# Performance work log

Measured on AMD Instinct MI355X. Metric: run time of the kernel, lower is better.

The kernel has to match this reference:

```python
import jax, jax.numpy as jnp
import numpy as np


def setup_inputs() -> dict:
    key = jax.random.key(0)
    ks = jax.random.split(key, 9)
    b, m, e, d = 4, 4096, 2048, 256
    s = 1.0 / np.sqrt(d)
    return {
        "features": jax.random.normal(ks[0], (b, m, d), jnp.float32),
        "inc_mat": (jax.random.uniform(ks[1], (b, m, e)) < 0.05).astype(jnp.float32),
        "vc_W_att": jax.random.normal(ks[2], (d, d), jnp.float32) * s,
        "vc_W_proj": jax.random.normal(ks[3], (d, d), jnp.float32) * s,
        "vc_alpha": jnp.float32(0.5),
        "ec_W_att": jax.random.normal(ks[4], (d, d), jnp.float32) * s,
        "ec_W_proj": jax.random.normal(ks[5], (d, d), jnp.float32) * s,
        "ec_alpha": jnp.float32(0.5),
        "n_layers": 3,
    }


def _vertex_conv(feat, inc, W_att, W_proj, alpha, prev_edge):
    # feat: [b,m,d], inc: [b,m,e]
    node_scores = jnp.einsum('bmd,kd->bmk', feat, W_att)          # attention Linear (x @ W.T)
    edge_scores = jnp.einsum('bme,bmd->bed', inc, node_scores)    # inc^T @ scores
    attn = jax.nn.softmax(edge_scores, axis=1)                    # softmax over edge dim (dim=1 in torch)
    # einsum('bme,bmd->bmed') then ('bmed,bed->bed') == attn * (inc^T @ feat); no 4D intermediate
    agg = jnp.einsum('bme,bmd->bed', inc, feat)
    ef = jnp.einsum('bed,kd->bek', attn * agg, W_proj)
    if prev_edge is not None:
        ef = alpha * prev_edge + (1.0 - alpha) * ef
    return ef


def _edge_conv(inc, edge_feats, W_proj, alpha, prev_node):
    # note: EdgeConv's attention softmax is computed but unused in the original forward
    weighted = jnp.einsum('bed,bme->bmd', edge_feats, inc)        # scatter edges back to nodes
    nf = jnp.einsum('bmd,kd->bmk', weighted, W_proj)
    if prev_node is not None:
        nf = alpha * prev_node + (1.0 - alpha) * nf
    return nf


def reference(features, inc_mat, vc_W_att, vc_W_proj, vc_alpha, ec_W_att, ec_W_proj, ec_alpha, n_layers):
    edge_feats = _vertex_conv(features, inc_mat, vc_W_att, vc_W_proj, vc_alpha, None)
    node_feats = _edge_conv(inc_mat, edge_feats, ec_W_proj, ec_alpha, features)
    for _ in range(1, int(n_layers)):
        edge_feats = _vertex_conv(features, inc_mat, vc_W_att, vc_W_proj, vc_alpha, edge_feats)
        node_feats = _edge_conv(inc_mat, edge_feats, ec_W_proj, ec_alpha, node_feats)
    return (node_feats, edge_feats, inc_mat)
```

## Files before the change

### kernel.cpp

```cpp
#include <hip/hip_runtime.h>
#include <hip/hip_bf16.h>
#include <math.h>

typedef __attribute__((ext_vector_type(8))) short s8v;
typedef __attribute__((ext_vector_type(4))) float f32x4;

__device__ __forceinline__ ushort f2bf(float x){ __hip_bfloat16 h = __float2bfloat16(x); return *(ushort*)&h; }
__device__ __forceinline__ float  bf2f(ushort u){ return __bfloat162float(*(__hip_bfloat16*)&u); }

template<int MAP> __device__ __forceinline__ int kmap(int k){
  if constexpr (MAP==0) return k;
  else if constexpr (MAP==1) return k & 4095;
  else if constexpr (MAP==3) return (((k>>8)&1)<<8) | (k&255);
  else if constexpr (MAP==4) return k & 255;
  else return (((k>>9)&1)<<8) | (k&255);
}

template<int AMAP, int BMAP, int EPI, int FR>
__global__ __launch_bounds__(256)
void gemm_kernel(const ushort* __restrict__ A, int lda, long long sA,
                 const ushort* __restrict__ B, int ldb, long long sB,
                 void* __restrict__ Cp, void* __restrict__ Cp2,
                 int ldc, long long sC, int ldc2, long long sC2,
                 long long kpC, int Kloc, int kparts,
                 const float* __restrict__ blend,
                 const float* __restrict__ alpha_p, const int* __restrict__ L_p)
{
  constexpr int BMt = 32*FR;
  __shared__ ushort As[BMt][40];
  __shared__ ushort Bs[BMt][40];

  const int z  = blockIdx.z;
  const int b  = z / kparts;
  const int kp = z - b*kparts;
  const int kbase = kp * Kloc;
  A += (size_t)b * sA;
  B += (size_t)b * sB;
  const int m0 = blockIdx.x * BMt;
  const int n0 = blockIdx.y * BMt;
  const int t = threadIdx.x, lane = t & 63, wid = t >> 6;
  const int wr = (wid>>1)*(16*FR), wc = (wid&1)*(16*FR);
  const int lrow = lane & 15, koff = (lane>>4)<<3;

  f32x4 acc[FR][FR];
  #pragma unroll
  for (int i=0;i<FR;i++)
    #pragma unroll
    for (int j=0;j<FR;j++) acc[i][j] = (f32x4)(0.f);

  for (int k0 = 0; k0 < Kloc; k0 += 32) {
    if constexpr (FR==4) {
      const int row = t>>1, cb = (t&1)*16;
      { const ushort* s = A + (size_t)(m0+row)*lda + kmap<AMAP>(kbase+k0+cb);
        *(s8v*)&As[row][cb] = *(const s8v*)s; *(s8v*)&As[row][cb+8] = *(const s8v*)(s+8); }
      { const ushort* s = B + (size_t)(n0+row)*ldb + kmap<BMAP>(kbase+k0+cb);
        *(s8v*)&Bs[row][cb] = *(const s8v*)s; *(s8v*)&Bs[row][cb+8] = *(const s8v*)(s+8); }
    } else {
      const int row = t>>2, cb = (t&3)*8;
      *(s8v*)&As[row][cb] = *(const s8v*)(A + (size_t)(m0+row)*lda + kmap<AMAP>(kbase+k0+cb));
      *(s8v*)&Bs[row][cb] = *(const s8v*)(B + (size_t)(n0+row)*ldb + kmap<BMAP>(kbase+k0+cb));
    }
    __syncthreads();
    s8v af[FR], bfv[FR];
    #pragma unroll
    for (int mi=0; mi<FR; mi++) af[mi]  = *(const s8v*)&As[wr+mi*16+lrow][koff];
    #pragma unroll
    for (int ni=0; ni<FR; ni++) bfv[ni] = *(const s8v*)&Bs[wc+ni*16+lrow][koff];
    #pragma unroll
    for (int mi=0; mi<FR; mi++)
      #pragma unroll
      for (int ni=0; ni<FR; ni++)
        acc[mi][ni] = __builtin_amdgcn_mfma_f32_16x16x32_bf16(af[mi], bfv[ni], acc[mi][ni], 0,0,0);
    __syncthreads();
  }

  float aL = 0.f;
  if constexpr (EPI==2) { aL = powf(*alpha_p, (float)(*L_p)); }
  const int cr = (lane>>4)<<2, cc = lane & 15;
  #pragma unroll
  for (int mi=0; mi<FR; mi++)
    #pragma unroll
    for (int ni=0; ni<FR; ni++) {
      const int row0 = m0 + wr + mi*16 + cr;
      const int col  = n0 + wc + ni*16 + cc;
      if constexpr (EPI==0) {
        float* C = (float*)Cp + kp*kpC + (size_t)b*sC;
        #pragma unroll
        for (int r=0;r<4;r++) C[(size_t)(row0+r)*ldc + col] = acc[mi][ni][r];
      } else if constexpr (EPI==1) {
        ushort* C = (ushort*)Cp + (size_t)b*sC;
        #pragma unroll
        for (int r=0;r<4;r++) C[(size_t)(row0+r)*ldc + col] = f2bf(acc[mi][ni][r]);
      } else if constexpr (EPI==2) {
        float* C = (float*)Cp + (size_t)b*sC;
        const float* bl = blend + (size_t)b*sC;
        #pragma unroll
        for (int r=0;r<4;r++) {
          const size_t idx = (size_t)(row0+r)*ldc + col;
          C[idx] = aL*bl[idx] + (1.f-aL)*acc[mi][ni][r];
        }
      } else if constexpr (EPI==6) {
        float* C = (float*)Cp + (size_t)b*sC;
        #pragma unroll
        for (int r=0;r<4;r++) C[(size_t)(row0+r)*ldc + col] = acc[mi][ni][r];
        float* C2 = (float*)Cp2 + (size_t)b*sC2 + (size_t)col*ldc2 + row0;
        *(f32x4*)C2 = acc[mi][ni];
      } else {
        float* C = (float*)Cp + (size_t)b*sC;
        #pragma unroll
        for (int r=0;r<4;r++) C[(size_t)(row0+r)*ldc + col] = acc[mi][ni][r];
        ushort4 o;
        o.x = f2bf(acc[mi][ni][0]); o.y = f2bf(acc[mi][ni][1]);
        o.z = f2bf(acc[mi][ni][2]); o.w = f2bf(acc[mi][ni][3]);
        *(ushort4*)((ushort*)Cp2 + (size_t)b*sC2 + (size_t)col*ldc2 + row0) = o;
      }
    }
}

__global__ __launch_bounds__(256)
void trans_inc_kernel(const float* __restrict__ src, float* __restrict__ outF32, int writeF32,
                      ushort* __restrict__ incbf, ushort* __restrict__ incT)
{
  __shared__ ushort T[64][65];
  const int b = blockIdx.z, m0 = blockIdx.x*64, e0 = blockIdx.y*64;
  const int t = threadIdx.x, rl = t>>2, cl = (t&3)*16;
  const size_t roff = (size_t)b*4096*2048 + (size_t)(m0+rl)*2048 + e0 + cl;
  const float* s = src + roff;
  ushort tmp[16] __attribute__((aligned(16)));
  float4 vv[4];
  #pragma unroll
  for (int i=0;i<4;i++) {
    vv[i] = ((const float4*)s)[i];
    tmp[4*i+0]=f2bf(vv[i].x); tmp[4*i+1]=f2bf(vv[i].y);
    tmp[4*i+2]=f2bf(vv[i].z); tmp[4*i+3]=f2bf(vv[i].w);
  }
  if (writeF32) {
    float4* o = (float4*)(outF32 + roff);
    #pragma unroll
    for (int i=0;i<4;i++) o[i] = vv[i];
  }
  ushort* d = incbf + roff;
  *(s8v*)d = *(s8v*)&tmp[0]; *(s8v*)(d+8) = *(s8v*)&tmp[8];
  #pragma unroll
  for (int j=0;j<16;j++) T[rl][cl+j] = tmp[j];
  __syncthreads();
  const int er = t>>2, mc = (t&3)*16;
  ushort o[16] __attribute__((aligned(16)));
  #pragma unroll
  for (int j=0;j<16;j++) o[j] = T[mc+j][er];
  ushort* d2 = incT + (size_t)b*2048*4096 + (size_t)(e0+er)*4096 + m0 + mc;
  *(s8v*)d2 = *(s8v*)&o[0]; *(s8v*)(d2+8) = *(s8v*)&o[8];
}

__global__ __launch_bounds__(256)
void trans_feat_kernel(const float* __restrict__ feat, ushort* __restrict__ fT)
{
  __shared__ ushort Th[64][65], Tl[64][65];
  const int b = blockIdx.z, m0 = blockIdx.x*64, d0 = blockIdx.y*64;
  const int t = threadIdx.x, rl = t>>2, cl = (t&3)*16;
  const float* s = feat + (size_t)b*4096*256 + (size_t)(m0+rl)*256 + d0 + cl;
  #pragma unroll
  for (int i=0;i<4;i++) {
    float4 v = ((const float4*)s)[i];
    float a[4] = {v.x,v.y,v.z,v.w};
    #pragma unroll
    for (int j=0;j<4;j++) {
      ushort h = f2bf(a[j]); Th[rl][cl+4*i+j] = h; Tl[rl][cl+4*i+j] = f2bf(a[j] - bf2f(h));
    }
  }
  __syncthreads();
  const int dr = t>>2, mc = (t&3)*16;
  ushort oh[16] __attribute__((aligned(16)));
  ushort ol[16] __attribute__((aligned(16)));
  #pragma unroll
  for (int j=0;j<16;j++) { oh[j] = Th[mc+j][dr]; ol[j] = Tl[mc+j][dr]; }
  ushort* d2 = fT + (size_t)b*256*8192 + (size_t)(d0+dr)*8192 + m0 + mc;
  *(s8v*)d2 = *(s8v*)&oh[0]; *(s8v*)(d2+8) = *(s8v*)&oh[8];
  *(s8v*)(d2+4096) = *(s8v*)&ol[0]; *(s8v*)(d2+4104) = *(s8v*)&ol[8];
}

__global__ __launch_bounds__(256)
void cvt_w_kernel(const float4* __restrict__ W, ushort* __restrict__ Ws)
{
  size_t i  = (size_t)blockIdx.x * 256 + threadIdx.x;
  size_t e0 = i * 4;
  int c = (int)(e0 & 255), r = (int)(e0 >> 8);
  float4 v = W[i];
  float a[4] = {v.x,v.y,v.z,v.w};
  ushort* hi = Ws + (size_t)r*512 + c;
  #pragma unroll
  for (int j=0;j<4;j++) { ushort h = f2bf(a[j]); hi[j] = h; hi[256+j] = f2bf(a[j]-bf2f(h)); }
}

__global__ __launch_bounds__(256)
void aggsum_kernel(const float* __restrict__ parts, long long kpC, int kparts,
                   ushort* __restrict__ AGGcat)
{
  const size_t i4 = (size_t)blockIdx.x*256 + threadIdx.x;
  float4 sv = make_float4(0.f,0.f,0.f,0.f);
  for (int kp=0; kp<kparts; kp++) {
    float4 v = ((const float4*)(parts + (size_t)kp*kpC))[i4];
    sv.x+=v.x; sv.y+=v.y; sv.z+=v.z; sv.w+=v.w;
  }
  const size_t flat = i4*4;
  const size_t row = flat >> 8;
  const int d = (int)(flat & 255);
  float a[4] = {sv.x, sv.y, sv.z, sv.w};
  ushort4 hi, lo;
  { ushort h=f2bf(a[0]); hi.x=h; lo.x=f2bf(a[0]-bf2f(h)); }
  { ushort h=f2bf(a[1]); hi.y=h; lo.y=f2bf(a[1]-bf2f(h)); }
  { ushort h=f2bf(a[2]); hi.z=h; lo.z=f2bf(a[2]-bf2f(h)); }
  { ushort h=f2bf(a[3]); hi.w=h; lo.w=f2bf(a[3]-bf2f(h)); }
  ushort* dst = AGGcat + row*512 + d;
  *(ushort4*)dst = hi; *(ushort4*)(dst+256) = lo;
}

__global__ __launch_bounds__(256)
void stats_kernel(const float* __restrict__ ESt, float2* __restrict__ stats)
{
  const int b = blockIdx.x >> 8, d = blockIdx.x & 255;
  const float* base = ESt + ((size_t)b*256 + d)*2048;
  const int t = threadIdx.x;
  const float4* p = (const float4*)base + t*2;
  float4 x = p[0], y = p[1];
  float v[8] = {x.x,x.y,x.z,x.w,y.x,y.y,y.z,y.w};
  float mx = v[0];
  #pragma unroll
  for (int j=1;j<8;j++) mx = fmaxf(mx, v[j]);
  #pragma unroll
  for (int off=32; off>=1; off>>=1) mx = fmaxf(mx, __shfl_down(mx, off));
  __shared__ float sm[8];
  const int lane = t & 63, w = t >> 6;
  if (lane==0) sm[w] = mx;
  __syncthreads();
  if (t==0) { sm[4] = fmaxf(fmaxf(sm[0],sm[1]),fmaxf(sm[2],sm[3])); }
  __syncthreads();
  mx = sm[4];
  float s = 0.f;
  #pragma unroll
  for (int j=0;j<8;j++) s += __expf(v[j]-mx);
  #pragma unroll
  for (int off=32; off>=1; off>>=1) s += __shfl_down(s, off);
  if (lane==0) sm[w] = s;
  __syncthreads();
  if (t==0) { float ss = sm[0]+sm[1]+sm[2]+sm[3]; stats[blockIdx.x] = make_float2(mx, 1.f/ss); }
}

__global__ __launch_bounds__(256)
void pmul_kernel(const float* __restrict__ ES, const ushort* __restrict__ AGGcat,
                 const float2* __restrict__ stats, ushort* __restrict__ P)
{
  const int b = blockIdx.x >> 6, e0 = (blockIdx.x & 63) * 32;
  const int t = threadIdx.x, tx = t & 63, ty = t >> 6;
  const int d4 = tx*4;
  const float2 st0 = stats[b*256+d4+0], st1 = stats[b*256+d4+1];
  const float2 st2 = stats[b*256+d4+2], st3 = stats[b*256+d4+3];
  for (int e = e0+ty; e < e0+32; e += 4) {
    const size_t ro = (size_t)b*2048 + e;
    float4 es = *(const float4*)(ES + ro*256 + d4);
    ushort4 ah = *(const ushort4*)(AGGcat + ro*512 + d4);
    ushort4 al = *(const ushort4*)(AGGcat + ro*512 + 256 + d4);
    ushort4 o;
    o.x = f2bf(__expf(es.x-st0.x)*st0.y*(bf2f(ah.x)+bf2f(al.x)));
    o.y = f2bf(__expf(es.y-st1.x)*st1.y*(bf2f(ah.y)+bf2f(al.y)));
    o.z = f2bf(__expf(es.z-st2.x)*st2.y*(bf2f(ah.z)+bf2f(al.z)));
    o.w = f2bf(__expf(es.w-st3.x)*st3.y*(bf2f(ah.w)+bf2f(al.w)));
    *(ushort4*)(P + ro*256 + d4) = o;
  }
}

__global__ __launch_bounds__(256)
void inc_copy_kernel(const float4* __restrict__ src, float4* __restrict__ dst, size_t n4)
{
  size_t i = (size_t)blockIdx.x*256 + threadIdx.x;
  const size_t stride = (size_t)gridDim.x*256;
  for (; i < n4; i += stride) dst[i] = src[i];
}

extern "C" void kernel_launch(void* const* d_in, const int* in_sizes, int n_in,
                              void* d_out, int out_size, void* d_ws, size_t ws_size,
                              hipStream_t stream) {
  const float* feat    = (const float*)d_in[0];
  const float* inc     = (const float*)d_in[1];
  const float* vcWatt  = (const float*)d_in[2];
  const float* vcWproj = (const float*)d_in[3];
  const float* ecWproj = (const float*)d_in[6];
  const float* ecAlpha = (const float*)d_in[7];
  const int*   nLayers = (const int*)d_in[8];

  const int Bb=4, Mm=4096, E=2048, D=256;
  const size_t nodeN = (size_t)Bb*Mm*D, edgeN = (size_t)Bb*E*D, incN = (size_t)Bb*Mm*E;

  const int kparts = 8;
  const size_t fTB    = (size_t)Bb*256*8192*2;
  const size_t partsB = (size_t)kparts*Bb*E*D*4;
  const size_t AGGcatB= (size_t)Bb*E*512*2;
  const size_t ESB    = (size_t)Bb*E*D*4;
  const size_t EStB   = ESB;
  const size_t PB     = edgeN*2;
  const size_t edgeTB = edgeN*2;
  const size_t WtB    = nodeN*2;
  const size_t WsB    = (size_t)3*256*512*2;
  const size_t statB  = (size_t)Bb*256*sizeof(float2);
  const size_t incTB  = incN*2, incbfB = incN*2;
  const size_t needB  = fTB+partsB+AGGcatB+ESB+EStB+PB+edgeTB+WtB+WsB+statB;
  const bool planA = ws_size >= needB + incTB + incbfB;

  char* ws = (char*)d_ws;
  ushort* fT    = (ushort*)ws;  ws += fTB;
  float*  parts = (float*)ws;   ws += partsB;
  ushort* AGGcat= (ushort*)ws;  ws += AGGcatB;
  float*  ES    = (float*)ws;   ws += ESB;
  float*  ESt   = (float*)ws;   ws += EStB;
  ushort* P     = (ushort*)ws;  ws += PB;
  ushort* edgeT = (ushort*)ws;  ws += edgeTB;
  ushort* Wt    = (ushort*)ws;  ws += WtB;
  ushort* Ws0   = (ushort*)ws;
  ushort* Ws1   = Ws0 + 256*512;
  ushort* Ws2   = Ws1 + 256*512;
  ws += WsB;
  float2* stats = (float2*)ws;  ws += statB;

  float* outNode = (float*)d_out;
  float* outEdge = outNode + nodeN;
  float* outInc  = outEdge + edgeN;
  ushort* incT, *incbf;
  if (planA) { incT = (ushort*)ws; incbf = incT + incN; }
  else       { incT = (ushort*)outInc; incbf = incT + incN; }

  const long long kpC = (long long)Bb*E*D;
  dim3 blk(256);

  cvt_w_kernel<<<dim3(64), blk, 0, stream>>>((const float4*)vcWatt,  Ws0);
  cvt_w_kernel<<<dim3(64), blk, 0, stream>>>((const float4*)vcWproj, Ws1);
  cvt_w_kernel<<<dim3(64), blk, 0, stream>>>((const float4*)ecWproj, Ws2);
  trans_feat_kernel<<<dim3(64,4,4), blk, 0, stream>>>(feat, fT);
  trans_inc_kernel<<<dim3(64,32,4), blk, 0, stream>>>(inc, outInc, planA ? 1 : 0, incbf, incT);

  gemm_kernel<1,0,0,4><<<dim3(16,2,4*kparts), blk, 0, stream>>>(
      incT, 4096, (long long)E*4096, fT, 8192, (long long)256*8192,
      parts, nullptr, D, (long long)E*D, 0, 0, kpC, 8192/kparts, kparts,
      nullptr, nullptr, nullptr);

  aggsum_kernel<<<dim3(2048), blk, 0, stream>>>(parts, kpC, kparts, AGGcat);

  gemm_kernel<5,3,6,2><<<dim3(32,4,4), blk, 0, stream>>>(
      AGGcat, 512, (long long)E*512, Ws0, 512, 0,
      ES, ESt, D, (long long)E*D, E, (long long)D*E, 0, 1024, 1,
      nullptr, nullptr, nullptr);

  stats_kernel<<<dim3(Bb*256), blk, 0, stream>>>(ESt, stats);
  pmul_kernel<<<dim3(Bb*64), blk, 0, stream>>>(ES, AGGcat, stats, P);

  gemm_kernel<4,3,7,2><<<dim3(32,4,4), blk, 0, stream>>>(
      P, 256, (long long)E*D, Ws1, 512, 0,
      outEdge, edgeT, D, (long long)E*D, E, (long long)D*E, 0, 512, 1,
      nullptr, nullptr, nullptr);

  gemm_kernel<0,0,1,2><<<dim3(64,4,4), blk, 0, stream>>>(
      incbf, 2048, (long long)Mm*E, edgeT, 2048, (long long)D*E,
      Wt, nullptr, D, (long long)Mm*D, 0, 0, 0, 2048, 1,
      nullptr, nullptr, nullptr);

  gemm_kernel<4,3,2,2><<<dim3(64,4,4), blk, 0, stream>>>(
      Wt, 256, (long long)Mm*D, Ws2, 512, 0,
      outNode, nullptr, D, (long long)Mm*D, 0, 0, 0, 512, 1,
      feat, ecAlpha, nLayers);

  if (!planA)
    inc_copy_kernel<<<dim3(2048), blk, 0, stream>>>((const float4*)inc, (float4*)outInc, incN/4);
}
```

Before: 527.5 us.

## Reassociate edge conv projection, load tiles via global_load_lds, reorder grid

The edge-side projection is reassociated: edge features are first multiplied by W_proj on the small edge dimension (E=2048), and the result is then scattered to nodes through the incidence matrix. This replaces a projection over M=4096 rows and drops the Wt intermediate. GEMM tile loads now use global_load_lds direct-to-LDS 16-byte loads with unpadded shared arrays, and the grid ordering is swapped so consecutive blocks share the A tile. Unpadded LDS may add bank conflicts on fragment reads, and the extra bf16 rounding of the projected edges changes numerics slightly.

```diff
diff --git a/kernel.cpp b/kernel.cpp
--- a/kernel.cpp
+++ b/kernel.cpp
@@ -7,6 +7,12 @@
 
 __device__ __forceinline__ ushort f2bf(float x){ __hip_bfloat16 h = __float2bfloat16(x); return *(ushort*)&h; }
 __device__ __forceinline__ float  bf2f(ushort u){ return __bfloat162float(*(__hip_bfloat16*)&u); }
+
+__device__ __forceinline__ void gload16(const void* g, void* l) {
+  __builtin_amdgcn_global_load_lds(
+      (const __attribute__((address_space(1))) void*)g,
+      (__attribute__((address_space(3))) void*)l, 16, 0, 0);
+}
 
 template<int MAP> __device__ __forceinline__ int kmap(int k){
   if constexpr (MAP==0) return k;
@@ -16,7 +22,7 @@
   else return (((k>>9)&1)<<8) | (k&255);
 }
 
-template<int AMAP, int BMAP, int EPI, int FR>
+template<int AMAP, int BMAP, int EPI, int FR, int GORD>
 __global__ __launch_bounds__(256)
 void gemm_kernel(const ushort* __restrict__ A, int lda, long long sA,
                  const ushort* __restrict__ B, int ldb, long long sB,
@@ -27,8 +33,8 @@
                  const float* __restrict__ alpha_p, const int* __restrict__ L_p)
 {
   constexpr int BMt = 32*FR;
-  __shared__ ushort As[BMt][40];
-  __shared__ ushort Bs[BMt][40];
+  __shared__ ushort As[BMt][32];
+  __shared__ ushort Bs[BMt][32];
 
   const int z  = blockIdx.z;
   const int b  = z / kparts;
@@ -36,11 +42,13 @@
   const int kbase = kp * Kloc;
   A += (size_t)b * sA;
   B += (size_t)b * sB;
-  const int m0 = blockIdx.x * BMt;
-  const int n0 = blockIdx.y * BMt;
+  const int m0 = (GORD ? blockIdx.x : blockIdx.y) * BMt;
+  const int n0 = (GORD ? blockIdx.y : blockIdx.x) * BMt;
   const int t = threadIdx.x, lane = t & 63, wid = t >> 6;
   const int wr = (wid>>1)*(16*FR), wc = (wid&1)*(16*FR);
   const int lrow = lane & 15, koff = (lane>>4)<<3;
+  const int rsub = lane >> 2;
+  const int kc   = (lane & 3) * 8;
 
   f32x4 acc[FR][FR];
   #pragma unroll
@@ -49,16 +57,11 @@
     for (int j=0;j<FR;j++) acc[i][j] = (f32x4)(0.f);
 
   for (int k0 = 0; k0 < Kloc; k0 += 32) {
-    if constexpr (FR==4) {
-      const int row = t>>1, cb = (t&1)*16;
-      { const ushort* s = A + (size_t)(m0+row)*lda + kmap<AMAP>(kbase+k0+cb);
-        *(s8v*)&As[row][cb] = *(const s8v*)s; *(s8v*)&As[row][cb+8] = *(const s8v*)(s+8); }
-      { const ushort* s = B + (size_t)(n0+row)*ldb + kmap<BMAP>(kbase+k0+cb);
-        *(s8v*)&Bs[row][cb] = *(const s8v*)s; *(s8v*)&Bs[row][cb+8] = *(const s8v*)(s+8); }
-    } else {
-      const int row = t>>2, cb = (t&3)*8;
-      *(s8v*)&As[row][cb] = *(const s8v*)(A + (size_t)(m0+row)*lda + kmap<AMAP>(kbase+k0+cb));
-      *(s8v*)&Bs[row][cb] = *(const s8v*)(B + (size_t)(n0+row)*ldb + kmap<BMAP>(kbase+k0+cb));
+    #pragma unroll
+    for (int c = wid; c < 2*FR; c += 4) {
+      const int row = c*16 + rsub;
+      gload16(A + (size_t)(m0+row)*lda + kmap<AMAP>(kbase+k0+kc), (char*)&As[0][0] + c*1024);
+      gload16(B + (size_t)(n0+row)*ldb + kmap<BMAP>(kbase+k0+kc), (char*)&Bs[0][0] + c*1024);
     }
     __syncthreads();
     s8v af[FR], bfv[FR];
@@ -87,10 +90,6 @@
         float* C = (float*)Cp + kp*kpC + (size_t)b*sC;
         #pragma unroll
         for (int r=0;r<4;r++) C[(size_t)(row0+r)*ldc + col] = acc[mi][ni][r];
-      } else if constexpr (EPI==1) {
-        ushort* C = (ushort*)Cp + (size_t)b*sC;
-        #pragma unroll
-        for (int r=0;r<4;r++) C[(size_t)(row0+r)*ldc + col] = f2bf(acc[mi][ni][r]);
       } else if constexpr (EPI==2) {
         float* C = (float*)Cp + (size_t)b*sC;
         const float* bl = blend + (size_t)b*sC;
@@ -99,6 +98,15 @@
           const size_t idx = (size_t)(row0+r)*ldc + col;
           C[idx] = aL*bl[idx] + (1.f-aL)*acc[mi][ni][r];
         }
+      } else if constexpr (EPI==3) {
+        float* C = (float*)Cp + (size_t)b*sC;
+        ushort* C2 = (ushort*)Cp2 + (size_t)b*sC;
+        #pragma unroll
+        for (int r=0;r<4;r++) {
+          const size_t idx = (size_t)(row0+r)*ldc + col;
+          C[idx] = acc[mi][ni][r];
+          C2[idx] = f2bf(acc[mi][ni][r]);
+        }
       } else if constexpr (EPI==6) {
         float* C = (float*)Cp + (size_t)b*sC;
         #pragma unroll
@@ -106,9 +114,6 @@
         float* C2 = (float*)Cp2 + (size_t)b*sC2 + (size_t)col*ldc2 + row0;
         *(f32x4*)C2 = acc[mi][ni];
       } else {
-        float* C = (float*)Cp + (size_t)b*sC;
-        #pragma unroll
-        for (int r=0;r<4;r++) C[(size_t)(row0+r)*ldc + col] = acc[mi][ni][r];
         ushort4 o;
         o.x = f2bf(acc[mi][ni][0]); o.y = f2bf(acc[mi][ni][1]);
         o.z = f2bf(acc[mi][ni][2]); o.w = f2bf(acc[mi][ni][3]);
@@ -298,12 +303,12 @@
   const size_t ESB    = (size_t)Bb*E*D*4;
   const size_t EStB   = ESB;
   const size_t PB     = edgeN*2;
-  const size_t edgeTB = edgeN*2;
-  const size_t WtB    = nodeN*2;
+  const size_t ebfB   = edgeN*2;
+  const size_t E2TB   = edgeN*2;
   const size_t WsB    = (size_t)3*256*512*2;
   const size_t statB  = (size_t)Bb*256*sizeof(float2);
   const size_t incTB  = incN*2, incbfB = incN*2;
-  const size_t needB  = fTB+partsB+AGGcatB+ESB+EStB+PB+edgeTB+WtB+WsB+statB;
+  const size_t needB  = fTB+partsB+AGGcatB+ESB+EStB+PB+ebfB+E2TB+WsB+statB;
   const bool planA = ws_size >= needB + incTB + incbfB;
 
   char* ws = (char*)d_ws;
@@ -313,8 +318,8 @@
   float*  ES    = (float*)ws;   ws += ESB;
   float*  ESt   = (float*)ws;   ws += EStB;
   ushort* P     = (ushort*)ws;  ws += PB;
-  ushort* edgeT = (ushort*)ws;  ws += edgeTB;
-  ushort* Wt    = (ushort*)ws;  ws += WtB;
+  ushort* edgebf= (ushort*)ws;  ws += ebfB;
+  ushort* E2T   = (ushort*)ws;  ws += E2TB;
   ushort* Ws0   = (ushort*)ws;
   ushort* Ws1   = Ws0 + 256*512;
   ushort* Ws2   = Ws1 + 256*512;
@@ -324,7 +329,7 @@
   float* outNode = (float*)d_out;
   float* outEdge = outNode + nodeN;
   float* outInc  = outEdge + edgeN;
-  ushort* incT, *incbf;
+  ushort *incT, *incbf;
   if (planA) { incT = (ushort*)ws; incbf = incT + incN; }
   else       { incT = (ushort*)outInc; incbf = incT + incN; }
 
@@ -337,14 +342,14 @@
   trans_feat_kernel<<<dim3(64,4,4), blk, 0, stream>>>(feat, fT);
   trans_inc_kernel<<<dim3(64,32,4), blk, 0, stream>>>(inc, outInc, planA ? 1 : 0, incbf, incT);
 
-  gemm_kernel<1,0,0,4><<<dim3(16,2,4*kparts), blk, 0, stream>>>(
+  gemm_kernel<1,0,0,4,0><<<dim3(2,16,4*kparts), blk, 0, stream>>>(
       incT, 4096, (long long)E*4096, fT, 8192, (long long)256*8192,
       parts, nullptr, D, (long long)E*D, 0, 0, kpC, 8192/kparts, kparts,
       nullptr, nullptr, nullptr);
 
   aggsum_kernel<<<dim3(2048), blk, 0, stream>>>(parts, kpC, kparts, AGGcat);
 
-  gemm_kernel<5,3,6,2><<<dim3(32,4,4), blk, 0, stream>>>(
+  gemm_kernel<5,3,6,2,0><<<dim3(4,32,4), blk, 0, stream>>>(
       AGGcat, 512, (long long)E*512, Ws0, 512, 0,
       ES, ESt, D, (long long)E*D, E, (long long)D*E, 0, 1024, 1,
       nullptr, nullptr, nullptr);
@@ -352,19 +357,19 @@
   stats_kernel<<<dim3(Bb*256), blk, 0, stream>>>(ESt, stats);
   pmul_kernel<<<dim3(Bb*64), blk, 0, stream>>>(ES, AGGcat, stats, P);
 
-  gemm_kernel<4,3,7,2><<<dim3(32,4,4), blk, 0, stream>>>(
+  gemm_kernel<4,3,3,2,0><<<dim3(4,32,4), blk, 0, stream>>>(
       P, 256, (long long)E*D, Ws1, 512, 0,
-      outEdge, edgeT, D, (long long)E*D, E, (long long)D*E, 0, 512, 1,
+      outEdge, edgebf, D, (long long)E*D, 0, 0, 0, 512, 1,
       nullptr, nullptr, nullptr);
 
-  gemm_kernel<0,0,1,2><<<dim3(64,4,4), blk, 0, stream>>>(
-      incbf, 2048, (long long)Mm*E, edgeT, 2048, (long long)D*E,
-      Wt, nullptr, D, (long long)Mm*D, 0, 0, 0, 2048, 1,
+  gemm_kernel<4,3,8,2,0><<<dim3(4,32,4), blk, 0, stream>>>(
+      edgebf, 256, (long long)E*D, Ws2, 512, 0,
+      nullptr, E2T, D, (long long)E*D, E, (long long)D*E, 0, 512, 1,
       nullptr, nullptr, nullptr);
 
-  gemm_kernel<4,3,2,2><<<dim3(64,4,4), blk, 0, stream>>>(
-      Wt, 256, (long long)Mm*D, Ws2, 512, 0,
-      outNode, nullptr, D, (long long)Mm*D, 0, 0, 0, 512, 1,
+  gemm_kernel<0,0,2,2,1><<<dim3(64,4,4), blk, 0, stream>>>(
+      incbf, 2048, (long long)Mm*E, E2T, 2048, (long long)D*E,
+      outNode, nullptr, D, (long long)Mm*D, 0, 0, 0, 2048, 1,
       feat, ecAlpha, nLayers);
 
   if (!planA)
```

After: 512.1 us. 1.03x faster.
